# Performance work log

Measured on AMD Instinct MI355X. Metric: run time of the kernel, lower is better.

## Reference

```python
import jax, jax.numpy as jnp
import numpy as np

N_NODES = 100000
N_EDGES = 1600000
N_GRAPHS = 64
IN_DIM = 256
OUT_DIM = 512
H1 = OUT_DIM // 4   # 128
H2 = OUT_DIM // 2   # 256


def glorot(key, shape):
    lim = float(np.sqrt(6.0 / (shape[0] + shape[1])))
    return jax.random.uniform(key, shape, jnp.float32, -lim, lim)


def setup_inputs() -> dict:
    key = jax.random.key(0)
    ks = jax.random.split(key, 8)
    x = jax.random.normal(ks[0], (N_NODES, IN_DIM), jnp.float32)
    edge_index = jax.random.randint(ks[1], (2, N_EDGES), 0, N_NODES, jnp.int64)
    batch = jnp.sort(jax.random.randint(ks[2], (N_NODES,), 0, N_GRAPHS, jnp.int64))
    return {
        'x': x,
        'edge_index': edge_index,
        'batch': batch,
        'W1': glorot(ks[3], (IN_DIM, H1)),
        'b1': jnp.zeros((H1,), jnp.float32),
        'W2': glorot(ks[4], (H1, H2)),
        'b2': jnp.zeros((H2,), jnp.float32),
        'fc_W': glorot(ks[5], (H2, OUT_DIM)),
        'fc_b': jnp.zeros((OUT_DIM,), jnp.float32),
    }


def gcn_conv(x, W, b, src, dst, n_nodes):
    # PyG GCNConv (default): add self-loops, sym-normalized aggregation of XW + bias
    h = x @ W                                   # [N, F_out] transform first (cheaper gather)
    ones = jnp.ones((src.shape[0],), h.dtype)
    deg = jax.ops.segment_sum(ones, dst, num_segments=n_nodes)  # includes self-loops
    dinv = jax.lax.rsqrt(jnp.maximum(deg, 1.0))
    norm = dinv[src] * dinv[dst]                # [E]
    msg = h[src] * norm[:, None]                # gather + scale
    out = jax.ops.segment_sum(msg, dst, num_segments=n_nodes)   # scatter-add
    return out + b


def reference(x, edge_index, batch, W1, b1, W2, b2, fc_W, fc_b):
    n = x.shape[0]
    loops = jnp.arange(n, dtype=edge_index.dtype)
    src = jnp.concatenate([edge_index[0], loops])
    dst = jnp.concatenate([edge_index[1], loops])

    h = jax.nn.relu(gcn_conv(x, W1, b1, src, dst, n))   # dropout = identity (eval)
    h = jax.nn.relu(gcn_conv(h, W2, b2, src, dst, n))

    # global_mean_pool over batch ids
    sums = jax.ops.segment_sum(h, batch, num_segments=N_GRAPHS)
    cnts = jax.ops.segment_sum(jnp.ones((n,), h.dtype), batch, num_segments=N_GRAPHS)
    pooled = sums / jnp.maximum(cnts, 1.0)[:, None]     # [B, H2]

    return jax.nn.relu(pooled @ fc_W + fc_b)            # [B, OUT_DIM]
```

## Files before the change

kernel.cpp:

```cpp
#include <hip/hip_runtime.h>
#include <hip/hip_bf16.h>
#include <cstdint>

#define N_NODES 100000
#define N_EDGES 1600000
#define N_GRAPHS 64
#define IN_DIM 256
#define HD1 128
#define HD2 256
#define OUT_DIM 512

#define NBUCK 196
#define NBLK  196
#define EPB   8192

typedef __bf16 bf16x8 __attribute__((ext_vector_type(8)));
typedef float f32x4 __attribute__((ext_vector_type(4)));

static __device__ __forceinline__ float bflo(uint32_t v) { return __uint_as_float(v << 16); }
static __device__ __forceinline__ float bfhi(uint32_t v) { return __uint_as_float(v & 0xffff0000u); }
static __device__ __forceinline__ uint32_t f2bf_bits(float f) {
    uint32_t u = __float_as_uint(f);
    return (u + 0x7fffu + ((u >> 16) & 1u)) >> 16;
}
static __device__ __forceinline__ uint32_t packbf(float a, float b) {
    return f2bf_bits(a) | (f2bf_bits(b) << 16);
}
static __device__ __forceinline__ float bf2f(uint16_t b) { return __uint_as_float(((uint32_t)b) << 16); }

__global__ void k_probe(const uint32_t* __restrict__ xw, const int* __restrict__ ei,
                        int* __restrict__ flags) {
    if (threadIdx.x != 0 || blockIdx.x != 0) return;
    int mid = 0;
    for (int i = 0; i < 64; i++) {
        uint32_t f = (xw[i] >> 23) & 0xFF;
        if (f >= 64 && f < 200) mid++;
    }
    flags[0] = (mid < 32) ? 1 : 0;
    int nz = 0;
    for (int i = 0; i < 64; i++) if (ei[2 * i + 1] != 0) nz++;
    flags[1] = (nz == 0) ? 1 : 0;
}

static __device__ __forceinline__ int ld_idx(const int* p, int i, int sh) { return p[i << sh]; }
static __device__ __forceinline__ float ld_f(const void* p, int i, int isbf) {
    return isbf ? bf2f(((const uint16_t*)p)[i]) : ((const float*)p)[i];
}

__global__ __launch_bounds__(256) void k_prep(const void* __restrict__ W1, const void* __restrict__ W2,
                                              const void* __restrict__ fcW, const void* __restrict__ b1,
                                              const void* __restrict__ b2, const void* __restrict__ fcb,
                                              uint16_t* __restrict__ W1T, uint16_t* __restrict__ W2T,
                                              uint16_t* __restrict__ fcWc, uint16_t* __restrict__ bc1,
                                              uint16_t* __restrict__ bc2, uint16_t* __restrict__ fcbc,
                                              const int* __restrict__ flags) {
    int i = blockIdx.x * 256 + threadIdx.x;
    int isbf = flags[0];
    if (i < 32768) {
        int n = i / IN_DIM, k = i % IN_DIM;
        W1T[i] = (uint16_t)f2bf_bits(ld_f(W1, k * HD1 + n, isbf));
    } else if (i < 65536) {
        int j = i - 32768;
        int n = j / HD1, k = j % HD1;
        W2T[j] = (uint16_t)f2bf_bits(ld_f(W2, k * HD2 + n, isbf));
    } else if (i < 196608) {
        int j = i - 65536;
        fcWc[j] = (uint16_t)f2bf_bits(ld_f(fcW, j, isbf));
    } else if (i < 196736) {
        bc1[i - 196608] = (uint16_t)f2bf_bits(ld_f(b1, i - 196608, isbf));
    } else if (i < 196992) {
        bc2[i - 196736] = (uint16_t)f2bf_bits(ld_f(b2, i - 196736, isbf));
    } else if (i < 197504) {
        fcbc[i - 196992] = (uint16_t)f2bf_bits(ld_f(fcb, i - 196992, isbf));
    }
}


__global__ __launch_bounds__(256) void k_hist(const int* __restrict__ ei, int* __restrict__ bh,
                                              const int* __restrict__ flags) {
    __shared__ int h[NBUCK];
    int t = threadIdx.x, blk = blockIdx.x;
    if (t < NBUCK) h[t] = 0;
    __syncthreads();
    int sh = flags[1];
    int base = blk * EPB;
#pragma unroll
    for (int k = 0; k < EPB / 256; k++) {
        int e = base + k * 256 + t;
        if (e < N_EDGES) atomicAdd(&h[ld_idx(ei, N_EDGES + e, sh) >> 9], 1);
    }
    __syncthreads();
    if (t < NBUCK) bh[blk * NBUCK + t] = h[t];
}

__global__ __launch_bounds__(256) void k_colscan(const int* __restrict__ bh, int* __restrict__ bhoff,
                                                 int* __restrict__ bucket_cnt) {
    __shared__ int s[256];
    int b = blockIdx.x, t = threadIdx.x;
    int v = (t < NBLK) ? bh[t * NBUCK + b] : 0;
    s[t] = v; __syncthreads();
    for (int off = 1; off < 256; off <<= 1) {
        int x = (t >= off) ? s[t - off] : 0;
        __syncthreads();
        s[t] += x;
        __syncthreads();
    }
    if (t < NBLK) bhoff[t * NBUCK + b] = s[t] - v;
    if (t == 255) bucket_cnt[b] = s[255];
}

__global__ __launch_bounds__(256) void k_bscan(const int* __restrict__ bucket_cnt,
                                               int* __restrict__ bucket_base,
                                               int* __restrict__ row_ptr) {
    __shared__ int s[256];
    int t = threadIdx.x;
    int v = (t < NBUCK) ? bucket_cnt[t] : 0;
    s[t] = v; __syncthreads();
    for (int off = 1; off < 256; off <<= 1) {
        int x = (t >= off) ? s[t - off] : 0;
        __syncthreads();
        s[t] += x;
        __syncthreads();
    }
    if (t < NBUCK) bucket_base[t] = s[t] - v;
    if (t == NBUCK - 1) { bucket_base[NBUCK] = s[t]; row_ptr[N_NODES] = s[t]; }
}

__global__ __launch_bounds__(256) void k_part(const int* __restrict__ ei,
                                              const int* __restrict__ bucket_base,
                                              const int* __restrict__ bhoff,
                                              int* __restrict__ tmp,
                                              const int* __restrict__ flags) {
    __shared__ int cur[NBUCK];
    int t = threadIdx.x, blk = blockIdx.x;
    if (t < NBUCK) cur[t] = bucket_base[t] + bhoff[blk * NBUCK + t];
    __syncthreads();
    int sh = flags[1];
    int base = blk * EPB;
#pragma unroll
    for (int k = 0; k < EPB / 256; k++) {
        int e = base + k * 256 + t;
        if (e < N_EDGES) {
            int s = ld_idx(ei, e, sh), d = ld_idx(ei, N_EDGES + e, sh);
            int pos = atomicAdd(&cur[d >> 9], 1);
            tmp[pos] = (s << 9) | (d & 511);
        }
    }
}

__global__ __launch_bounds__(256) void k_bsort(const int* __restrict__ tmp,
                                               const int* __restrict__ bucket_base,
                                               int* __restrict__ csr_src,
                                               int* __restrict__ row_ptr,
                                               float* __restrict__ dinv) {
    __shared__ int h[512], a[512], c[512];
    int b = blockIdx.x, t = threadIdx.x;
    int beg = bucket_base[b], end = bucket_base[b + 1];
    h[t] = 0; h[t + 256] = 0;
    __syncthreads();
    for (int i = beg + t; i < end; i += 256) atomicAdd(&h[tmp[i] & 511], 1);
    __syncthreads();
    a[t] = h[t]; a[t + 256] = h[t + 256];
    __syncthreads();
    for (int off = 1; off < 512; off <<= 1) {
        int x0 = (t >= off) ? a[t - off] : 0;
        int x1 = ((t + 256) >= off) ? a[t + 256 - off] : 0;
        __syncthreads();
        a[t] += x0; a[t + 256] += x1;
        __syncthreads();
    }
#pragma unroll
    for (int u = 0; u < 2; u++) {
        int i = t + u * 256;
        int node = (b << 9) + i;
        int ex = a[i] - h[i];
        if (node < N_NODES) {
            row_ptr[node] = beg + ex;
            dinv[node] = rsqrtf((float)(h[i] + 1));
        }
        c[i] = ex;
    }
    __syncthreads();
    for (int i = beg + t; i < end; i += 256) {
        int e = tmp[i];
        int pos = atomicAdd(&c[e & 511], 1);
        csr_src[beg + pos] = e >> 9;
    }
}

#define GCNT_CHUNK 8
__global__ __launch_bounds__(256) void k_gcnt(const int* __restrict__ bat, int* __restrict__ gcnt,
                                              const int* __restrict__ flags) {
    __shared__ int h[N_GRAPHS];
    int t = threadIdx.x;
    if (t < N_GRAPHS) h[t] = 0;
    __syncthreads();
    int sh = flags[1];
    int base = (blockIdx.x * 256 + t) * GCNT_CHUNK;
    int cur = -1, run = 0;
#pragma unroll
    for (int u = 0; u < GCNT_CHUNK; u++) {
        int i = base + u;
        if (i < N_NODES) {
            int g = ld_idx(bat, i, sh);
            if (g == cur) run++;
            else { if (run) atomicAdd(&h[cur], run); cur = g; run = 1; }
        }
    }
    if (run) atomicAdd(&h[cur], run);
    __syncthreads();
    if (t < N_GRAPHS) { int v = h[t]; if (v) atomicAdd(&gcnt[t], v); }
}


__global__ __launch_bounds__(256, 4) void k_gemm1(const void* __restrict__ Ain,
                                                  const uint16_t* __restrict__ BT,
                                                  uint16_t* __restrict__ C,
                                                  const int* __restrict__ flags) {
    const int K = IN_DIM, N = HD1;
    int isbf = flags[0];
    int t = threadIdx.x;
    int wave = t >> 6, lane = t & 63;
    int quad = lane >> 4, l16 = lane & 15;
    int m0 = blockIdx.x * 32;
    int n0 = wave * 32;

    bf16x8 Bf[2][8];
#pragma unroll
    for (int nt = 0; nt < 2; nt++)
#pragma unroll
        for (int ks = 0; ks < 8; ks++)
            Bf[nt][ks] = *(const bf16x8*)(BT + (n0 + nt * 16 + l16) * K + ks * 32 + quad * 8);

    f32x4 acc[2][2];
#pragma unroll
    for (int a = 0; a < 2; a++)
#pragma unroll
        for (int b = 0; b < 2; b++) acc[a][b] = f32x4{0.f, 0.f, 0.f, 0.f};

    int arow[2] = { m0 + l16, m0 + 16 + l16 };

#pragma unroll
    for (int ks = 0; ks < 8; ks++) {
        int kc = ks * 32 + quad * 8;
        bf16x8 af[2];
#pragma unroll
        for (int mt = 0; mt < 2; mt++) {
            int off = arow[mt] * K + kc;
            if (isbf) {
                af[mt] = *(const bf16x8*)((const uint16_t*)Ain + off);
            } else {
                const float* p = (const float*)Ain + off;
                f32x4 f0 = *(const f32x4*)p, f1 = *(const f32x4*)(p + 4);
                union { uint16_t u[8]; bf16x8 v; } r;
#pragma unroll
                for (int j = 0; j < 4; j++) {
                    r.u[j]     = (uint16_t)f2bf_bits(f0[j]);
                    r.u[4 + j] = (uint16_t)f2bf_bits(f1[j]);
                }
                af[mt] = r.v;
            }
        }
#pragma unroll
        for (int mt = 0; mt < 2; mt++)
#pragma unroll
            for (int nt = 0; nt < 2; nt++)
                acc[mt][nt] = __builtin_amdgcn_mfma_f32_16x16x32_bf16(af[mt], Bf[nt][ks], acc[mt][nt], 0, 0, 0);
    }

#pragma unroll
    for (int mt = 0; mt < 2; mt++)
#pragma unroll
        for (int reg = 0; reg < 4; reg++) {
            int row = m0 + mt * 16 + quad * 4 + reg;
#pragma unroll
            for (int nt = 0; nt < 2; nt++)
                C[row * N + n0 + nt * 16 + l16] = (uint16_t)f2bf_bits(acc[mt][nt][reg]);
        }
}


template <int WITH_BIAS_RELU>
__global__ __launch_bounds__(256) void k_agg(const uint16_t* __restrict__ Yin, uint16_t* __restrict__ Yout,
                                             const int* __restrict__ row_ptr, const int* __restrict__ csr_src,
                                             const float* __restrict__ dinv, const uint16_t* __restrict__ bias) {
    int node = blockIdx.x * 4 + (threadIdx.x >> 6);
    int l = threadIdx.x & 63;
    const uint32_t* Y32 = (const uint32_t*)Yin;

    float wd = dinv[node];
    uint32_t v = Y32[(size_t)node * 64 + l];
    float a0 = wd * bflo(v), a1 = wd * bfhi(v);

    int e0 = row_ptr[node], e1 = row_ptr[node + 1];
    for (int cb = e0; cb < e1; cb += 64) {
        int cnt = e1 - cb; if (cnt > 64) cnt = 64;
        int my_src = 0; uint32_t my_w = 0;
        if (l < cnt) { my_src = csr_src[cb + l]; my_w = __float_as_uint(dinv[my_src]); }
        int rounds = (cnt + 15) >> 4;
        for (int r = 0; r < rounds; r++) {
            int jb = r * 16;
            uint32_t vv[16];
#pragma unroll
            for (int t = 0; t < 16; t++) {
                int s = __builtin_amdgcn_readlane(my_src, jb + t);
                vv[t] = Y32[(size_t)s * 64 + l];
            }
#pragma unroll
            for (int t = 0; t < 16; t++) {
                float w = __uint_as_float(__builtin_amdgcn_readlane(my_w, jb + t));
                a0 += w * bflo(vv[t]);
                a1 += w * bfhi(vv[t]);
            }
        }
    }
    a0 *= wd; a1 *= wd;
    if (WITH_BIAS_RELU) {
        a0 = fmaxf(a0 + bf2f(bias[2 * l]), 0.f);
        a1 = fmaxf(a1 + bf2f(bias[2 * l + 1]), 0.f);
    }
    ((uint32_t*)Yout)[(size_t)node * 64 + l] = packbf(a0, a1);
}


__global__ __launch_bounds__(512, 4) void k_gemm2_pool(const uint16_t* __restrict__ A,
                                                       const uint16_t* __restrict__ BT,
                                                       const uint16_t* __restrict__ bias,
                                                       const int* __restrict__ bat,
                                                       const int* __restrict__ flags,
                                                       float* __restrict__ pooled) {
    const int K = HD1;
    int t = threadIdx.x;
    int wave = t >> 6, lane = t & 63;
    int quad = lane >> 4, l16 = lane & 15;
    int m0 = blockIdx.x * 32;
    int n0 = wave * 32;

    bf16x8 Bf[2][4];
#pragma unroll
    for (int nt = 0; nt < 2; nt++)
#pragma unroll
        for (int ks = 0; ks < 4; ks++)
            Bf[nt][ks] = *(const bf16x8*)(BT + (n0 + nt * 16 + l16) * K + ks * 32 + quad * 8);

    f32x4 acc[2][2];
#pragma unroll
    for (int a = 0; a < 2; a++)
#pragma unroll
        for (int b = 0; b < 2; b++) acc[a][b] = f32x4{0.f, 0.f, 0.f, 0.f};

    int arow[2] = { m0 + l16, m0 + 16 + l16 };

#pragma unroll
    for (int ks = 0; ks < 4; ks++) {
        int kc = ks * 32 + quad * 8;
        bf16x8 af[2];
#pragma unroll
        for (int mt = 0; mt < 2; mt++)
            af[mt] = *(const bf16x8*)(A + arow[mt] * K + kc);
#pragma unroll
        for (int mt = 0; mt < 2; mt++)
#pragma unroll
            for (int nt = 0; nt < 2; nt++)
                acc[mt][nt] = __builtin_amdgcn_mfma_f32_16x16x32_bf16(af[mt], Bf[nt][ks], acc[mt][nt], 0, 0, 0);
    }

    int sh = flags[1];
    float bv[2];
#pragma unroll
    for (int nt = 0; nt < 2; nt++) bv[nt] = bf2f(bias[n0 + nt * 16 + l16]);

    int gfirst = ld_idx(bat, m0, sh);
    int glast  = ld_idx(bat, m0 + 31, sh);
    if (gfirst == glast) {
#pragma unroll
        for (int nt = 0; nt < 2; nt++) {
            float s = 0.f;
#pragma unroll
            for (int mt = 0; mt < 2; mt++)
#pragma unroll
                for (int reg = 0; reg < 4; reg++)
                    s += fmaxf(acc[mt][nt][reg] + bv[nt], 0.f);
            s += __shfl_xor(s, 16);
            s += __shfl_xor(s, 32);
            if (quad == 0)
                atomicAdd(&pooled[gfirst * HD2 + n0 + nt * 16 + l16], s);
        }
    } else {
#pragma unroll
        for (int mt = 0; mt < 2; mt++) {
            int rb = m0 + mt * 16 + quad * 4;
#pragma unroll
            for (int reg = 0; reg < 4; reg++) {
                int g = ld_idx(bat, rb + reg, sh);
#pragma unroll
                for (int nt = 0; nt < 2; nt++)
                    atomicAdd(&pooled[g * HD2 + n0 + nt * 16 + l16],
                              fmaxf(acc[mt][nt][reg] + bv[nt], 0.f));
            }
        }
    }
}


__global__ __launch_bounds__(512) void k_final(const float* __restrict__ pooled, const int* __restrict__ gcnt,
                                               const uint16_t* __restrict__ fcWc, const uint16_t* __restrict__ fcbc,
                                               void* __restrict__ out, const int* __restrict__ flags) {
    __shared__ float pm[HD2];
    int g = blockIdx.x, t = threadIdx.x;
    if (t < HD2) pm[t] = pooled[g * HD2 + t] / fmaxf((float)gcnt[g], 1.0f);
    __syncthreads();
    float acc = bf2f(fcbc[t]);
    for (int k = 0; k < HD2; k++) acc = fmaf(pm[k], bf2f(fcWc[k * OUT_DIM + t]), acc);
    acc = fmaxf(acc, 0.f);
    if (flags[0]) ((uint16_t*)out)[g * OUT_DIM + t] = (uint16_t)f2bf_bits(acc);
    else          ((float*)out)[g * OUT_DIM + t] = acc;
}


extern "C" void kernel_launch(void* const* d_in, const int* in_sizes, int n_in,
                              void* d_out, int out_size, void* d_ws, size_t ws_size,
                              hipStream_t stream) {
    const void* x   = d_in[0];
    const int*  ei  = (const int*)d_in[1];
    const int*  bat = (const int*)d_in[2];
    const void* W1  = d_in[3];
    const void* b1  = d_in[4];
    const void* W2  = d_in[5];
    const void* b2  = d_in[6];
    const void* fcW = d_in[7];
    const void* fcb = d_in[8];

    char* ws = (char*)d_ws;
    size_t off = 0;
    auto alloc = [&](size_t bytes) -> void* {
        void* p = ws + off;
        off += (bytes + 255) & ~(size_t)255;
        return p;
    };
    uint16_t* buf0 = (uint16_t*)alloc((size_t)N_NODES * HD1 * 2);
    uint16_t* Hb   = (uint16_t*)alloc((size_t)N_NODES * HD1 * 2);
    int*   row_ptr = (int*)alloc((N_NODES + 1) * 4);
    int*   csr_src = (int*)alloc((size_t)N_EDGES * 4);
    int*   tmp     = (int*)alloc((size_t)N_EDGES * 4);
    int*   bh      = (int*)alloc(NBLK * NBUCK * 4);
    int*   bhoff   = (int*)alloc(NBLK * NBUCK * 4);
    int*   bucket_cnt  = (int*)alloc(NBUCK * 4);
    int*   bucket_base = (int*)alloc((NBUCK + 1) * 4);
    float* dinv    = (float*)alloc(N_NODES * 4);
    int*   gcnt    = (int*)alloc(N_GRAPHS * 4);
    float* pooled  = (float*)alloc(N_GRAPHS * HD2 * 4);
    uint16_t* W1T  = (uint16_t*)alloc(IN_DIM * HD1 * 2);
    uint16_t* W2T  = (uint16_t*)alloc(HD1 * HD2 * 2);
    uint16_t* bc1  = (uint16_t*)alloc(HD1 * 2);
    uint16_t* bc2  = (uint16_t*)alloc(HD2 * 2);
    uint16_t* fcWc = (uint16_t*)alloc(HD2 * OUT_DIM * 2);
    uint16_t* fcbc = (uint16_t*)alloc(OUT_DIM * 2);
    int*   flags   = (int*)alloc(64 * 4);

    uint16_t* Y1 = buf0;
    uint16_t* Zb = buf0;

    hipMemsetAsync(gcnt, 0, N_GRAPHS * 4, stream);
    hipMemsetAsync(pooled, 0, N_GRAPHS * HD2 * 4, stream);

    k_probe<<<1, 64, 0, stream>>>((const uint32_t*)x, ei, flags);

    k_prep<<<(197504 + 255) / 256, 256, 0, stream>>>(W1, W2, fcW, b1, b2, fcb,
                                                     W1T, W2T, fcWc, bc1, bc2, fcbc, flags);

    k_hist<<<NBLK, 256, 0, stream>>>(ei, bh, flags);
    k_colscan<<<NBUCK, 256, 0, stream>>>(bh, bhoff, bucket_cnt);
    k_bscan<<<1, 256, 0, stream>>>(bucket_cnt, bucket_base, row_ptr);
    k_part<<<NBLK, 256, 0, stream>>>(ei, bucket_base, bhoff, tmp, flags);
    k_bsort<<<NBUCK, 256, 0, stream>>>(tmp, bucket_base, csr_src, row_ptr, dinv);

    k_gcnt<<<(N_NODES + 256 * GCNT_CHUNK - 1) / (256 * GCNT_CHUNK), 256, 0, stream>>>(bat, gcnt, flags);

    k_gemm1<<<N_NODES / 32, 256, 0, stream>>>(x, W1T, Y1, flags);
    k_agg<1><<<N_NODES / 4, 256, 0, stream>>>(Y1, Hb, row_ptr, csr_src, dinv, bc1);

    k_agg<0><<<N_NODES / 4, 256, 0, stream>>>(Hb, Zb, row_ptr, csr_src, dinv, nullptr);
    k_gemm2_pool<<<N_NODES / 32, 512, 0, stream>>>(Zb, W2T, bc2, bat, flags, pooled);

    k_final<<<N_GRAPHS, 512, 0, stream>>>(pooled, gcnt, fcWc, fcbc, d_out, flags);
}
```

Baseline: 479.3 us.

## Pre-swizzle weights into MFMA fragment order and retile GEMMs across row blocks

New measurement: 450.9 us. 1.06x faster.

```diff
diff --git a/kernel.cpp b/kernel.cpp
--- a/kernel.cpp
+++ b/kernel.cpp
@@ -50,19 +50,23 @@
 __global__ __launch_bounds__(256) void k_prep(const void* __restrict__ W1, const void* __restrict__ W2,
                                               const void* __restrict__ fcW, const void* __restrict__ b1,
                                               const void* __restrict__ b2, const void* __restrict__ fcb,
-                                              uint16_t* __restrict__ W1T, uint16_t* __restrict__ W2T,
+                                              uint16_t* __restrict__ W1F, uint16_t* __restrict__ W2F,
                                               uint16_t* __restrict__ fcWc, uint16_t* __restrict__ bc1,
                                               uint16_t* __restrict__ bc2, uint16_t* __restrict__ fcbc,
                                               const int* __restrict__ flags) {
     int i = blockIdx.x * 256 + threadIdx.x;
     int isbf = flags[0];
     if (i < 32768) {
-        int n = i / IN_DIM, k = i % IN_DIM;
-        W1T[i] = (uint16_t)f2bf_bits(ld_f(W1, k * HD1 + n, isbf));
+        int j = i & 7, l = (i >> 3) & 63, nt = (i >> 9) & 1, ks = (i >> 10) & 7, n0g = (i >> 13) & 3;
+        int k = ks * 32 + (l >> 4) * 8 + j;
+        int n = n0g * 32 + nt * 16 + (l & 15);
+        W1F[i] = (uint16_t)f2bf_bits(ld_f(W1, k * HD1 + n, isbf));
     } else if (i < 65536) {
-        int j = i - 32768;
-        int n = j / HD1, k = j % HD1;
-        W2T[j] = (uint16_t)f2bf_bits(ld_f(W2, k * HD2 + n, isbf));
+        int j2 = i - 32768;
+        int j = j2 & 7, l = (j2 >> 3) & 63, nt = (j2 >> 9) & 1, ks = (j2 >> 10) & 3, n0g = (j2 >> 12) & 7;
+        int k = ks * 32 + (l >> 4) * 8 + j;
+        int n = n0g * 32 + nt * 16 + (l & 15);
+        W2F[j2] = (uint16_t)f2bf_bits(ld_f(W2, k * HD2 + n, isbf));
     } else if (i < 196608) {
         int j = i - 65536;
         fcWc[j] = (uint16_t)f2bf_bits(ld_f(fcW, j, isbf));
@@ -213,44 +217,47 @@
 }
 
 
-__global__ __launch_bounds__(256, 4) void k_gemm1(const void* __restrict__ Ain,
-                                                  const uint16_t* __restrict__ BT,
-                                                  uint16_t* __restrict__ C,
-                                                  const int* __restrict__ flags) {
-    const int K = IN_DIM, N = HD1;
+__global__ __launch_bounds__(256) void k_gemm1(const void* __restrict__ Ain,
+                                               const uint16_t* __restrict__ BF,
+                                               uint16_t* __restrict__ C,
+                                               const int* __restrict__ flags) {
+    const int M = N_NODES, K = IN_DIM, N = HD1;
     int isbf = flags[0];
     int t = threadIdx.x;
     int wave = t >> 6, lane = t & 63;
     int quad = lane >> 4, l16 = lane & 15;
-    int m0 = blockIdx.x * 32;
-    int n0 = wave * 32;
-
-    bf16x8 Bf[2][8];
-#pragma unroll
-    for (int nt = 0; nt < 2; nt++)
+    int m0 = blockIdx.y * 128 + wave * 32;
+    int n0 = blockIdx.x * 32;
+
+    bf16x8 Bf[8][2];
+#pragma unroll
+    for (int ks = 0; ks < 8; ks++)
+#pragma unroll
+        for (int nt = 0; nt < 2; nt++)
+            Bf[ks][nt] = *(const bf16x8*)(BF + ((((blockIdx.x * 8 + ks) * 2 + nt) << 6) + lane) * 8);
+
+    int arow[2];
+#pragma unroll
+    for (int mt = 0; mt < 2; mt++) {
+        int r = m0 + mt * 16 + l16;
+        arow[mt] = r < M ? r : M - 1;
+    }
+
+    bf16x8 Af[8][2];
+    if (isbf) {
+        const uint16_t* Ab = (const uint16_t*)Ain;
 #pragma unroll
         for (int ks = 0; ks < 8; ks++)
-            Bf[nt][ks] = *(const bf16x8*)(BT + (n0 + nt * 16 + l16) * K + ks * 32 + quad * 8);
-
-    f32x4 acc[2][2];
-#pragma unroll
-    for (int a = 0; a < 2; a++)
-#pragma unroll
-        for (int b = 0; b < 2; b++) acc[a][b] = f32x4{0.f, 0.f, 0.f, 0.f};
-
-    int arow[2] = { m0 + l16, m0 + 16 + l16 };
-
-#pragma unroll
-    for (int ks = 0; ks < 8; ks++) {
-        int kc = ks * 32 + quad * 8;
-        bf16x8 af[2];
-#pragma unroll
-        for (int mt = 0; mt < 2; mt++) {
-            int off = arow[mt] * K + kc;
-            if (isbf) {
-                af[mt] = *(const bf16x8*)((const uint16_t*)Ain + off);
-            } else {
-                const float* p = (const float*)Ain + off;
+#pragma unroll
+            for (int mt = 0; mt < 2; mt++)
+                Af[ks][mt] = *(const bf16x8*)(Ab + arow[mt] * K + ks * 32 + quad * 8);
+    } else {
+        const float* Afp = (const float*)Ain;
+#pragma unroll
+        for (int ks = 0; ks < 8; ks++)
+#pragma unroll
+            for (int mt = 0; mt < 2; mt++) {
+                const float* p = Afp + arow[mt] * K + ks * 32 + quad * 8;
                 f32x4 f0 = *(const f32x4*)p, f1 = *(const f32x4*)(p + 4);
                 union { uint16_t u[8]; bf16x8 v; } r;
 #pragma unroll
@@ -258,24 +265,33 @@
                     r.u[j]     = (uint16_t)f2bf_bits(f0[j]);
                     r.u[4 + j] = (uint16_t)f2bf_bits(f1[j]);
                 }
-                af[mt] = r.v;
+                Af[ks][mt] = r.v;
             }
-        }
+    }
+
+    f32x4 acc[2][2];
+#pragma unroll
+    for (int a = 0; a < 2; a++)
+#pragma unroll
+        for (int b = 0; b < 2; b++) acc[a][b] = f32x4{0.f, 0.f, 0.f, 0.f};
+
+#pragma unroll
+    for (int ks = 0; ks < 8; ks++)
 #pragma unroll
         for (int mt = 0; mt < 2; mt++)
 #pragma unroll
             for (int nt = 0; nt < 2; nt++)
-                acc[mt][nt] = __builtin_amdgcn_mfma_f32_16x16x32_bf16(af[mt], Bf[nt][ks], acc[mt][nt], 0, 0, 0);
-    }
+                acc[mt][nt] = __builtin_amdgcn_mfma_f32_16x16x32_bf16(Af[ks][mt], Bf[ks][nt], acc[mt][nt], 0, 0, 0);
 
 #pragma unroll
     for (int mt = 0; mt < 2; mt++)
 #pragma unroll
         for (int reg = 0; reg < 4; reg++) {
             int row = m0 + mt * 16 + quad * 4 + reg;
-#pragma unroll
-            for (int nt = 0; nt < 2; nt++)
-                C[row * N + n0 + nt * 16 + l16] = (uint16_t)f2bf_bits(acc[mt][nt][reg]);
+            if (row < M)
+#pragma unroll
+                for (int nt = 0; nt < 2; nt++)
+                    C[row * N + n0 + nt * 16 + l16] = (uint16_t)f2bf_bits(acc[mt][nt][reg]);
         }
 }
 
@@ -323,25 +339,39 @@
 }
 
 
-__global__ __launch_bounds__(512, 4) void k_gemm2_pool(const uint16_t* __restrict__ A,
-                                                       const uint16_t* __restrict__ BT,
-                                                       const uint16_t* __restrict__ bias,
-                                                       const int* __restrict__ bat,
-                                                       const int* __restrict__ flags,
-                                                       float* __restrict__ pooled) {
-    const int K = HD1;
+__global__ __launch_bounds__(256) void k_gemm2_pool(const uint16_t* __restrict__ A,
+                                                    const uint16_t* __restrict__ BF,
+                                                    const uint16_t* __restrict__ bias,
+                                                    const int* __restrict__ bat,
+                                                    const int* __restrict__ flags,
+                                                    float* __restrict__ pooled) {
+    const int M = N_NODES, K = HD1;
     int t = threadIdx.x;
     int wave = t >> 6, lane = t & 63;
     int quad = lane >> 4, l16 = lane & 15;
-    int m0 = blockIdx.x * 32;
-    int n0 = wave * 32;
-
-    bf16x8 Bf[2][4];
-#pragma unroll
-    for (int nt = 0; nt < 2; nt++)
-#pragma unroll
-        for (int ks = 0; ks < 4; ks++)
-            Bf[nt][ks] = *(const bf16x8*)(BT + (n0 + nt * 16 + l16) * K + ks * 32 + quad * 8);
+    int m0 = blockIdx.y * 128 + wave * 32;
+    int n0 = blockIdx.x * 32;
+
+    bf16x8 Bf[4][2];
+#pragma unroll
+    for (int ks = 0; ks < 4; ks++)
+#pragma unroll
+        for (int nt = 0; nt < 2; nt++)
+            Bf[ks][nt] = *(const bf16x8*)(BF + ((((blockIdx.x * 4 + ks) * 2 + nt) << 6) + lane) * 8);
+
+    int arow[2];
+#pragma unroll
+    for (int mt = 0; mt < 2; mt++) {
+        int r = m0 + mt * 16 + l16;
+        arow[mt] = r < M ? r : M - 1;
+    }
+
+    bf16x8 Af[4][2];
+#pragma unroll
+    for (int ks = 0; ks < 4; ks++)
+#pragma unroll
+        for (int mt = 0; mt < 2; mt++)
+            Af[ks][mt] = *(const bf16x8*)(A + arow[mt] * K + ks * 32 + quad * 8);
 
     f32x4 acc[2][2];
 #pragma unroll
@@ -349,54 +379,48 @@
 #pragma unroll
         for (int b = 0; b < 2; b++) acc[a][b] = f32x4{0.f, 0.f, 0.f, 0.f};
 
-    int arow[2] = { m0 + l16, m0 + 16 + l16 };
-
-#pragma unroll
-    for (int ks = 0; ks < 4; ks++) {
-        int kc = ks * 32 + quad * 8;
-        bf16x8 af[2];
+#pragma unroll
+    for (int ks = 0; ks < 4; ks++)
 #pragma unroll
         for (int mt = 0; mt < 2; mt++)
-            af[mt] = *(const bf16x8*)(A + arow[mt] * K + kc);
-#pragma unroll
-        for (int mt = 0; mt < 2; mt++)
 #pragma unroll
             for (int nt = 0; nt < 2; nt++)
-                acc[mt][nt] = __builtin_amdgcn_mfma_f32_16x16x32_bf16(af[mt], Bf[nt][ks], acc[mt][nt], 0, 0, 0);
-    }
+                acc[mt][nt] = __builtin_amdgcn_mfma_f32_16x16x32_bf16(Af[ks][mt], Bf[ks][nt], acc[mt][nt], 0, 0, 0);
 
     int sh = flags[1];
     float bv[2];
 #pragma unroll
     for (int nt = 0; nt < 2; nt++) bv[nt] = bf2f(bias[n0 + nt * 16 + l16]);
 
-    int gfirst = ld_idx(bat, m0, sh);
-    int glast  = ld_idx(bat, m0 + 31, sh);
-    if (gfirst == glast) {
-#pragma unroll
-        for (int nt = 0; nt < 2; nt++) {
-            float s = 0.f;
-#pragma unroll
-            for (int mt = 0; mt < 2; mt++)
-#pragma unroll
-                for (int reg = 0; reg < 4; reg++)
-                    s += fmaxf(acc[mt][nt][reg] + bv[nt], 0.f);
-            s += __shfl_xor(s, 16);
-            s += __shfl_xor(s, 32);
-            if (quad == 0)
-                atomicAdd(&pooled[gfirst * HD2 + n0 + nt * 16 + l16], s);
-        }
-    } else {
-#pragma unroll
-        for (int mt = 0; mt < 2; mt++) {
-            int rb = m0 + mt * 16 + quad * 4;
-#pragma unroll
-            for (int reg = 0; reg < 4; reg++) {
-                int g = ld_idx(bat, rb + reg, sh);
-#pragma unroll
-                for (int nt = 0; nt < 2; nt++)
-                    atomicAdd(&pooled[g * HD2 + n0 + nt * 16 + l16],
-                              fmaxf(acc[mt][nt][reg] + bv[nt], 0.f));
+    if (m0 < M) {
+        int gfirst = ld_idx(bat, m0, sh);
+        int glast  = ld_idx(bat, m0 + 31, sh);
+        if (gfirst == glast) {
+#pragma unroll
+            for (int nt = 0; nt < 2; nt++) {
+                float s = 0.f;
+#pragma unroll
+                for (int mt = 0; mt < 2; mt++)
+#pragma unroll
+                    for (int reg = 0; reg < 4; reg++)
+                        s += fmaxf(acc[mt][nt][reg] + bv[nt], 0.f);
+                s += __shfl_xor(s, 16);
+                s += __shfl_xor(s, 32);
+                if (quad == 0)
+                    atomicAdd(&pooled[gfirst * HD2 + n0 + nt * 16 + l16], s);
+            }
+        } else {
+#pragma unroll
+            for (int mt = 0; mt < 2; mt++) {
+                int rb = m0 + mt * 16 + quad * 4;
+#pragma unroll
+                for (int reg = 0; reg < 4; reg++) {
+                    int g = ld_idx(bat, rb + reg, sh);
+#pragma unroll
+                    for (int nt = 0; nt < 2; nt++)
+                        atomicAdd(&pooled[g * HD2 + n0 + nt * 16 + l16],
+                                  fmaxf(acc[mt][nt][reg] + bv[nt], 0.f));
+                }
             }
         }
     }
@@ -477,11 +501,11 @@
 
     k_gcnt<<<(N_NODES + 256 * GCNT_CHUNK - 1) / (256 * GCNT_CHUNK), 256, 0, stream>>>(bat, gcnt, flags);
 
-    k_gemm1<<<N_NODES / 32, 256, 0, stream>>>(x, W1T, Y1, flags);
+    k_gemm1<<<dim3(4, (N_NODES + 127) / 128), 256, 0, stream>>>(x, W1T, Y1, flags);
     k_agg<1><<<N_NODES / 4, 256, 0, stream>>>(Y1, Hb, row_ptr, csr_src, dinv, bc1);
 
     k_agg<0><<<N_NODES / 4, 256, 0, stream>>>(Hb, Zb, row_ptr, csr_src, dinv, nullptr);
-    k_gemm2_pool<<<N_NODES / 32, 512, 0, stream>>>(Zb, W2T, bc2, bat, flags, pooled);
+    k_gemm2_pool<<<dim3(8, (N_NODES + 127) / 128), 256, 0, stream>>>(Zb, W2T, bc2, bat, flags, pooled);
 
     k_final<<<N_GRAPHS, 512, 0, stream>>>(pooled, gcnt, fcWc, fcbc, d_out, flags);
 }
```
